# Kernel optimization log

Hardware: AMD Instinct MI355X
Metric: run time of the kernel (lower is better)

Reference implementation:

```python
import jax, jax.numpy as jnp
import numpy as np

N = 100000
E = 1600000
D_IN = 256
N_HEADS = 4
OUT_SZ = 32  # output_dim // n_heads = 128 // 4
ALPHA = 0.2  # leaky relu slope


def setup_inputs() -> dict:
    key = jax.random.key(0)
    ks = jax.random.split(key, 8)
    x = jax.random.normal(ks[0], (N, D_IN), dtype=jnp.float32)
    edge_row = jax.random.randint(ks[1], (E,), 0, N, dtype=jnp.int32)
    edge_col = jax.random.randint(ks[2], (E,), 0, N, dtype=jnp.int32)
    # per-head params: W (conv1d k=1, no bias), a1/a2 (conv1d k=1 with bias)
    W = jax.random.normal(ks[3], (N_HEADS, D_IN, OUT_SZ), dtype=jnp.float32) * (1.0 / np.sqrt(D_IN))
    a1 = jax.random.normal(ks[4], (N_HEADS, OUT_SZ), dtype=jnp.float32) * (1.0 / np.sqrt(OUT_SZ))
    b1 = jnp.zeros((N_HEADS,), dtype=jnp.float32)
    a2 = jax.random.normal(ks[5], (N_HEADS, OUT_SZ), dtype=jnp.float32) * (1.0 / np.sqrt(OUT_SZ))
    b2 = jnp.zeros((N_HEADS,), dtype=jnp.float32)
    return {"x": x, "W": W, "a1": a1, "b1": b1, "a2": a2, "b2": b2,
            "edge_row": edge_row, "edge_col": edge_col}


def _gat_heads(x, W, a1, b1, a2, b2, edge_row, edge_col):
    # per-head linear transform: [H, N, O]
    fts = jnp.einsum('nd,hdo->hno', x, W)
    f1 = jnp.einsum('hno,ho->hn', fts, a1) + b1[:, None]  # [H, N]
    f2 = jnp.einsum('hno,ho->hn', fts, a2) + b2[:, None]  # [H, N]
    # edge logits: f1[row] + f2[col]  (adj values are 1)
    logits = f1[:, edge_row] + f2[:, edge_col]            # [H, E]
    lr = jnp.maximum(ALPHA * logits, logits)
    # segment softmax over each node's incoming edge set (rows)
    seg_max = jax.vmap(lambda v: jax.ops.segment_max(v, edge_row, num_segments=N))(lr)
    ex = jnp.exp(lr - seg_max[:, edge_row])
    denom = jax.vmap(lambda v: jax.ops.segment_sum(v, edge_row, num_segments=N))(ex)
    coef = ex / denom[:, edge_row]                        # [H, E]
    # SpMM aggregation: out[h, i] = sum_{e: row(e)=i} coef[h,e] * fts[h, col(e)]
    msg = coef[:, :, None] * fts[:, edge_col, :]          # [H, E, O]
    agg = jax.vmap(lambda m: jax.ops.segment_sum(m, edge_row, num_segments=N))(msg)  # [H, N, O]
    h = jnp.transpose(agg, (1, 0, 2)).reshape(N, N_HEADS * OUT_SZ)  # concat heads
    return jax.nn.elu(h)[None]  # [1, N, output_dim]


def reference(x, W, a1, b1, a2, b2, edge_row, edge_col):
    return _gat_heads(x, W, a1, b1, a2, b2, edge_row, edge_col)
```

## Files before the change

### kernel.cpp

```cpp
#include <hip/hip_runtime.h>
#include <hip/hip_bf16.h>
#include <math.h>

#define ALPHA 0.2f
#define PB_EDGES 4096

typedef __attribute__((ext_vector_type(8))) short short8;
typedef __attribute__((ext_vector_type(4))) float floatx4;

__device__ __forceinline__ ushort f2bf(float f) {
    uint u = __float_as_uint(f);
    u += 0x7fff + ((u >> 16) & 1);
    return (ushort)(u >> 16);
}

__global__ __launch_bounds__(256) void k_wprep(const float* __restrict__ W,
                                               ushort* __restrict__ Wt)
{
    int g = blockIdx.x * 256 + threadIdx.x;
    int c = g >> 8, d = g & 255;
    Wt[g] = f2bf(W[(c >> 5) * 8192 + d * 32 + (c & 31)]);
}

__global__ __launch_bounds__(256) void k_gemm(const float* __restrict__ x,
                                              const ushort* __restrict__ Wt,
                                              const float* __restrict__ a1v,
                                              const float* __restrict__ b1v,
                                              const float* __restrict__ a2v,
                                              const float* __restrict__ b2v,
                                              ushort* __restrict__ fts2,
                                              float* __restrict__ f1,
                                              float* __restrict__ f2, int M)
{
    __shared__ __align__(16) ushort smem[64 * 264];
    const int t  = threadIdx.x;
    const int m0 = blockIdx.x * 64;

#pragma unroll
    for (int i = 0; i < 16; i++) {
        int idx = i * 256 + t;
        int row = idx >> 6, c4 = idx & 63;
        int gr = m0 + row;
        float4 v = make_float4(0.f, 0.f, 0.f, 0.f);
        if (gr < M) v = *(const float4*)(x + (size_t)gr * 256 + c4 * 4);
        ushort4 b;
        b.x = f2bf(v.x); b.y = f2bf(v.y); b.z = f2bf(v.z); b.w = f2bf(v.w);
        *(ushort4*)&smem[row * 264 + c4 * 4] = b;
    }
    __syncthreads();

    const int w = t >> 6, lane = t & 63;
    const int mm = lane & 15, qq = lane >> 4;

    floatx4 acc[8];
#pragma unroll
    for (int ct = 0; ct < 8; ct++) acc[ct] = (floatx4){0.f, 0.f, 0.f, 0.f};

    const ushort* arow = &smem[(16 * w + mm) * 264 + qq * 8];
#pragma unroll
    for (int ks = 0; ks < 8; ks++) {
        short8 a8 = *(const short8*)(arow + ks * 32);
#pragma unroll
        for (int ct = 0; ct < 8; ct++) {
            short8 b8 = *(const short8*)(Wt + (ct * 16 + mm) * 256 + ks * 32 + qq * 8);
            acc[ct] = __builtin_amdgcn_mfma_f32_16x16x32_bf16(a8, b8, acc[ct], 0, 0, 0);
        }
    }

    __syncthreads();
    ushort* ftsL = smem;
#pragma unroll
    for (int ct = 0; ct < 8; ct++) {
#pragma unroll
        for (int i = 0; i < 4; i++) {
            int row = 16 * w + qq * 4 + i;
            ftsL[row * 136 + ct * 16 + mm] = f2bf(acc[ct][i]);
        }
    }
    __syncthreads();

    {
        int row = t >> 2, q4 = t & 3;
        int gr = m0 + row;
        if (gr < M) {
            const uint4* src = (const uint4*)&ftsL[row * 136 + q4 * 32];
            uint4* dst = (uint4*)(fts2 + (size_t)gr * 128 + q4 * 32);
            dst[0] = src[0];
            dst[1] = src[1];
            dst[2] = src[2];
            dst[3] = src[3];
        }
    }
    {
        int row = t >> 2, h = t & 3;
        int gr = m0 + row;
        if (gr < M) {
            const ushort* fr = &ftsL[row * 136 + h * 32];
            float s1 = 0.f, s2 = 0.f;
#pragma unroll
            for (int o = 0; o < 32; o++) {
                float v = __uint_as_float((uint)fr[o] << 16);
                s1 = fmaf(v, a1v[h * 32 + o], s1);
                s2 = fmaf(v, a2v[h * 32 + o], s2);
            }
            f1[gr * 4 + h] = s1 + b1v[h];
            f2[gr * 4 + h] = s2 + b2v[h];
        }
    }
}

__global__ __launch_bounds__(256) void k_phist(const int* __restrict__ erow,
                                               int* __restrict__ bcnt, int E, int NB)
{
    __shared__ int h[512];
    for (int i = threadIdx.x; i < 512; i += 256) h[i] = 0;
    __syncthreads();
    int b0 = blockIdx.x * PB_EDGES;
    int bend = b0 + PB_EDGES; if (bend > E) bend = E;
    for (int j = b0 + threadIdx.x; j < bend; j += 256)
        atomicAdd(&h[erow[j] >> 8], 1);
    __syncthreads();
    for (int i = threadIdx.x; i < NB; i += 256)
        if (h[i]) atomicAdd(&bcnt[i], h[i]);
}

__global__ __launch_bounds__(256) void k_scan_buckets(const int* __restrict__ bcnt,
                                                      int* __restrict__ base,
                                                      int* __restrict__ bcursor,
                                                      int NB, int E)
{
    __shared__ int s[256];
    int t = threadIdx.x;
    int i0 = 2 * t, i1 = 2 * t + 1;
    int v0 = (i0 < NB) ? bcnt[i0] : 0;
    int v1 = (i1 < NB) ? bcnt[i1] : 0;
    int tsum = v0 + v1;
    s[t] = tsum;
    __syncthreads();
    for (int off = 1; off < 256; off <<= 1) {
        int u = (t >= off) ? s[t - off] : 0;
        __syncthreads();
        s[t] += u;
        __syncthreads();
    }
    int excl = s[t] - tsum;
    if (i0 < NB) { base[i0] = excl;      bcursor[i0] = excl; }
    if (i1 < NB) { base[i1] = excl + v0; bcursor[i1] = excl + v0; }
    if (t == 0) base[NB] = E;
}

__global__ __launch_bounds__(256) void k_pscatter(const int* __restrict__ erow,
                                                  const int* __restrict__ ecol,
                                                  int* __restrict__ bcursor,
                                                  uint* __restrict__ part, int E)
{
    __shared__ int h[512];
    __shared__ int cur[512];
    for (int i = threadIdx.x; i < 512; i += 256) h[i] = 0;
    __syncthreads();
    int b0 = blockIdx.x * PB_EDGES;
    int bend = b0 + PB_EDGES; if (bend > E) bend = E;
    for (int j = b0 + threadIdx.x; j < bend; j += 256)
        atomicAdd(&h[erow[j] >> 8], 1);
    __syncthreads();
    for (int i = threadIdx.x; i < 512; i += 256)
        cur[i] = h[i] ? atomicAdd(&bcursor[i], h[i]) : 0;
    __syncthreads();
    for (int j = b0 + threadIdx.x; j < bend; j += 256) {
        int r = erow[j], c = ecol[j];
        int p = atomicAdd(&cur[r >> 8], 1);
        part[p] = ((uint)(r & 255) << 24) | (uint)c;
    }
}

__global__ __launch_bounds__(256) void k_bucket(const uint* __restrict__ part,
                                                const int* __restrict__ base,
                                                int* __restrict__ row_start,
                                                int* __restrict__ col_sorted,
                                                int Nn, int NB, int E)
{
    __shared__ int cnt[256];
    __shared__ int s[256];
    __shared__ int cur[256];
    const int b = blockIdx.x, t = threadIdx.x;
    const int start = base[b], end = base[b + 1];

    cnt[t] = 0;
    __syncthreads();
    for (int j = start + t; j < end; j += 256)
        atomicAdd(&cnt[part[j] >> 24], 1);
    __syncthreads();
    int v = cnt[t];
    s[t] = v;
    __syncthreads();
    for (int off = 1; off < 256; off <<= 1) {
        int u = (t >= off) ? s[t - off] : 0;
        __syncthreads();
        s[t] += u;
        __syncthreads();
    }
    int excl = s[t] - v;
    int r = b * 256 + t;
    if (r < Nn) row_start[r] = start + excl;
    if (b == 0 && t == 0) row_start[Nn] = E;
    cur[t] = start + excl;
    __syncthreads();
    for (int j = start + t; j < end; j += 256) {
        uint rc = part[j];
        int p = atomicAdd(&cur[rc >> 24], 1);
        col_sorted[p] = (int)(rc & 0xffffffu);
    }
}

__global__ __launch_bounds__(256) void k_gat_row(const ushort* __restrict__ fts2,
                                                 const float4* __restrict__ f1,
                                                 const float4* __restrict__ f2,
                                                 const int* __restrict__ row_start,
                                                 const int* __restrict__ cols,
                                                 float* __restrict__ out, int Nn)
{
    __shared__ float eL[4][256];
    __shared__ int   cL[4][64];

    const int wid  = threadIdx.x >> 6;
    const int lane = threadIdx.x & 63;
    const int r = blockIdx.x * 4 + wid;
    if (r >= Nn) return;

    const int s = row_start[r], e = row_start[r + 1];
    const int hl = lane >> 4;

    float2* outp = (float2*)(out + (size_t)r * 128);
    if (s == e) { outp[lane] = make_float2(0.f, 0.f); return; }

    const float4 f1r = f1[r];
    float ds0 = 0.f, ds1 = 0.f, ds2 = 0.f, ds3 = 0.f;
    float acc0 = 0.f, acc1 = 0.f;

    for (int j0 = s; j0 < e; j0 += 64) {
        int j = j0 + lane;
        bool act = (j < e);
        int c = act ? cols[j] : 0;
        float4 f2v = f2[c];
        float l0 = f1r.x + f2v.x; l0 = fmaxf(l0, ALPHA * l0);
        float l1 = f1r.y + f2v.y; l1 = fmaxf(l1, ALPHA * l1);
        float l2 = f1r.z + f2v.z; l2 = fmaxf(l2, ALPHA * l2);
        float l3 = f1r.w + f2v.w; l3 = fmaxf(l3, ALPHA * l3);
        float e0 = act ? __expf(l0) : 0.f;
        float e1 = act ? __expf(l1) : 0.f;
        float e2 = act ? __expf(l2) : 0.f;
        float e3 = act ? __expf(l3) : 0.f;
        ds0 += e0; ds1 += e1; ds2 += e2; ds3 += e3;

        asm volatile("s_waitcnt lgkmcnt(0)" ::: "memory");
        ((float4*)eL[wid])[lane] = make_float4(e0, e1, e2, e3);
        cL[wid][lane] = c;
        asm volatile("s_waitcnt lgkmcnt(0)" ::: "memory");

        int len = e - j0; if (len > 64) len = 64;
#pragma unroll 4
        for (int jj = 0; jj < len; jj++) {
            float ee = eL[wid][jj * 4 + hl];
            int   cc = cL[wid][jj];
            const uint* fp = (const uint*)(fts2 + (size_t)cc * 128);
            uint vv = fp[lane];
            float vx = __uint_as_float(vv << 16);
            float vy = __uint_as_float(vv & 0xffff0000u);
            acc0 = fmaf(ee, vx, acc0);
            acc1 = fmaf(ee, vy, acc1);
        }
    }

#pragma unroll
    for (int off = 32; off > 0; off >>= 1) {
        ds0 += __shfl_xor(ds0, off, 64);
        ds1 += __shfl_xor(ds1, off, 64);
        ds2 += __shfl_xor(ds2, off, 64);
        ds3 += __shfl_xor(ds3, off, 64);
    }
    float dsel = (hl == 0) ? ds0 : (hl == 1) ? ds1 : (hl == 2) ? ds2 : ds3;

    float o0 = acc0 / dsel;
    float o1 = acc1 / dsel;
    o0 = (o0 > 0.f) ? o0 : (__expf(o0) - 1.0f);
    o1 = (o1 > 0.f) ? o1 : (__expf(o1) - 1.0f);
    outp[lane] = make_float2(o0, o1);
}

extern "C" void kernel_launch(void* const* d_in, const int* in_sizes, int n_in,
                              void* d_out, int out_size, void* d_ws, size_t ws_size,
                              hipStream_t stream)
{
    const float* x   = (const float*)d_in[0];
    const float* W   = (const float*)d_in[1];
    const float* a1  = (const float*)d_in[2];
    const float* b1  = (const float*)d_in[3];
    const float* a2  = (const float*)d_in[4];
    const float* b2  = (const float*)d_in[5];
    const int*   erow = (const int*)d_in[6];
    const int*   ecol = (const int*)d_in[7];
    float* out = (float*)d_out;

    const int N = in_sizes[0] / 256;
    const int E = in_sizes[6];
    const int NB = (N + 255) >> 8;

    char*  ws  = (char*)d_ws;
    size_t off = 0;
    auto carve = [&](size_t bytes) -> char* {
        char* p = ws + off;
        off += (bytes + 255) & ~(size_t)255;
        return p;
    };
    ushort* fts2      = (ushort*)carve((size_t)N * 128 * 2);
    ushort* Wt        = (ushort*)carve((size_t)128 * 256 * 2);
    float*  f1        = (float*)carve((size_t)N * 4 * 4);
    float*  f2        = (float*)carve((size_t)N * 4 * 4);
    int*    row_start = (int*)carve(((size_t)N + 1) * 4);
    int*    bcnt      = (int*)carve(512 * 4);
    int*    base      = (int*)carve(513 * 4);
    int*    bcursor   = (int*)carve(512 * 4);
    int*    col_sorted= (int*)carve((size_t)E * 4);
    uint*   part      = (uint*)carve((size_t)E * 4);
    (void)ws_size;

    k_wprep<<<128, 256, 0, stream>>>(W, Wt);
    k_gemm<<<(N + 63) / 64, 256, 0, stream>>>(x, Wt, a1, b1, a2, b2, fts2, f1, f2, N);

    hipMemsetAsync(bcnt, 0, 512 * 4, stream);
    int npb = (E + PB_EDGES - 1) / PB_EDGES;
    k_phist<<<npb, 256, 0, stream>>>(erow, bcnt, E, NB);
    k_scan_buckets<<<1, 256, 0, stream>>>(bcnt, base, bcursor, NB, E);
    k_pscatter<<<npb, 256, 0, stream>>>(erow, ecol, bcursor, part, E);
    k_bucket<<<NB, 256, 0, stream>>>(part, base, row_start, col_sorted, N, NB, E);

    k_gat_row<<<(N + 3) / 4, 256, 0, stream>>>(fts2, (const float4*)f1, (const float4*)f2,
                                               row_start, col_sorted, out, N);
}
```

Measured before the change: 382.4 us.

## Stage W in LDS and load x fragments directly into registers in GEMM

The GEMM kernel now processes 128 rows per block instead of 64. It stages the bf16 weight matrix in shared memory in MFMA fragment order, and each wave computes two 16-row tiles that reuse each B fragment. A fragments are loaded straight from global fp32 x into registers and converted there, skipping the LDS round trip for x. This cuts repeated global W reads and LDS traffic, at the cost of higher register use (two accumulator sets plus 16 A fragments), which may lower occupancy.

```diff
diff --git a/kernel.cpp b/kernel.cpp
--- a/kernel.cpp
+++ b/kernel.cpp
@@ -12,6 +12,15 @@
     uint u = __float_as_uint(f);
     u += 0x7fff + ((u >> 16) & 1);
     return (ushort)(u >> 16);
+}
+
+__device__ __forceinline__ short8 pack8(float4 lo, float4 hi) {
+    short8 r;
+    r[0] = (short)f2bf(lo.x); r[1] = (short)f2bf(lo.y);
+    r[2] = (short)f2bf(lo.z); r[3] = (short)f2bf(lo.w);
+    r[4] = (short)f2bf(hi.x); r[5] = (short)f2bf(hi.y);
+    r[6] = (short)f2bf(hi.z); r[7] = (short)f2bf(hi.w);
+    return r;
 }
 
 __global__ __launch_bounds__(256) void k_wprep(const float* __restrict__ W,
@@ -32,70 +41,87 @@
                                               float* __restrict__ f1,
                                               float* __restrict__ f2, int M)
 {
-    __shared__ __align__(16) ushort smem[64 * 264];
+    __shared__ __align__(16) ushort smem[32768];
     const int t  = threadIdx.x;
-    const int m0 = blockIdx.x * 64;
+    const int m0 = blockIdx.x * 128;
 
 #pragma unroll
     for (int i = 0; i < 16; i++) {
-        int idx = i * 256 + t;
-        int row = idx >> 6, c4 = idx & 63;
-        int gr = m0 + row;
-        float4 v = make_float4(0.f, 0.f, 0.f, 0.f);
-        if (gr < M) v = *(const float4*)(x + (size_t)gr * 256 + c4 * 4);
-        ushort4 b;
-        b.x = f2bf(v.x); b.y = f2bf(v.y); b.z = f2bf(v.z); b.w = f2bf(v.w);
-        *(ushort4*)&smem[row * 264 + c4 * 4] = b;
-    }
-    __syncthreads();
+        int f = i * 256 + t;
+        int lane_ = f & 63, ksct = f >> 6;
+        int ks = ksct & 7, ct = ksct >> 3;
+        int mm = lane_ & 15, qq = lane_ >> 4;
+        *(uint4*)&smem[f * 8] = *(const uint4*)&Wt[(ct * 16 + mm) * 256 + ks * 32 + qq * 8];
+    }
 
     const int w = t >> 6, lane = t & 63;
     const int mm = lane & 15, qq = lane >> 4;
 
-    floatx4 acc[8];
-#pragma unroll
-    for (int ct = 0; ct < 8; ct++) acc[ct] = (floatx4){0.f, 0.f, 0.f, 0.f};
-
-    const ushort* arow = &smem[(16 * w + mm) * 264 + qq * 8];
+    int row0 = m0 + w * 32 + mm;
+    int row1 = row0 + 16;
+    int r0c = (row0 < M) ? row0 : (M - 1);
+    int r1c = (row1 < M) ? row1 : (M - 1);
+    const float* ar0 = x + (size_t)r0c * 256 + qq * 8;
+    const float* ar1 = x + (size_t)r1c * 256 + qq * 8;
+    short8 afrag[2][8];
 #pragma unroll
     for (int ks = 0; ks < 8; ks++) {
-        short8 a8 = *(const short8*)(arow + ks * 32);
+        float4 lo0 = *(const float4*)(ar0 + ks * 32);
+        float4 hi0 = *(const float4*)(ar0 + ks * 32 + 4);
+        float4 lo1 = *(const float4*)(ar1 + ks * 32);
+        float4 hi1 = *(const float4*)(ar1 + ks * 32 + 4);
+        afrag[0][ks] = pack8(lo0, hi0);
+        afrag[1][ks] = pack8(lo1, hi1);
+    }
+
+    floatx4 acc[2][8];
+#pragma unroll
+    for (int r = 0; r < 2; r++)
+#pragma unroll
+        for (int ct = 0; ct < 8; ct++) acc[r][ct] = (floatx4){0.f, 0.f, 0.f, 0.f};
+
+    __syncthreads();
+
+#pragma unroll
+    for (int ks = 0; ks < 8; ks++) {
 #pragma unroll
         for (int ct = 0; ct < 8; ct++) {
-            short8 b8 = *(const short8*)(Wt + (ct * 16 + mm) * 256 + ks * 32 + qq * 8);
-            acc[ct] = __builtin_amdgcn_mfma_f32_16x16x32_bf16(a8, b8, acc[ct], 0, 0, 0);
+            short8 b8 = *(const short8*)&smem[((ct * 8 + ks) * 64 + lane) * 8];
+            acc[0][ct] = __builtin_amdgcn_mfma_f32_16x16x32_bf16(afrag[0][ks], b8, acc[0][ct], 0, 0, 0);
+            acc[1][ct] = __builtin_amdgcn_mfma_f32_16x16x32_bf16(afrag[1][ks], b8, acc[1][ct], 0, 0, 0);
         }
     }
 
     __syncthreads();
     ushort* ftsL = smem;
 #pragma unroll
-    for (int ct = 0; ct < 8; ct++) {
-#pragma unroll
-        for (int i = 0; i < 4; i++) {
-            int row = 16 * w + qq * 4 + i;
-            ftsL[row * 136 + ct * 16 + mm] = f2bf(acc[ct][i]);
+    for (int r = 0; r < 2; r++)
+#pragma unroll
+        for (int ct = 0; ct < 8; ct++)
+#pragma unroll
+            for (int i = 0; i < 4; i++) {
+                int rowl = w * 32 + r * 16 + qq * 4 + i;
+                ftsL[rowl * 136 + ct * 16 + mm] = f2bf(acc[r][ct][i]);
+            }
+    __syncthreads();
+
+    {
+        int rowl = t >> 1, half = t & 1;
+        int gr = m0 + rowl;
+        if (gr < M) {
+            const uint4* src = (const uint4*)&ftsL[rowl * 136 + half * 64];
+            uint4* dst = (uint4*)(fts2 + (size_t)gr * 128 + half * 64);
+#pragma unroll
+            for (int i = 0; i < 8; i++) dst[i] = src[i];
         }
     }
-    __syncthreads();
-
-    {
-        int row = t >> 2, q4 = t & 3;
-        int gr = m0 + row;
+#pragma unroll
+    for (int p = 0; p < 2; p++) {
+        int task = p * 256 + t;
+        int rowl = task >> 2, h = task & 3;
+        int gr = m0 + rowl;
         if (gr < M) {
-            const uint4* src = (const uint4*)&ftsL[row * 136 + q4 * 32];
-            uint4* dst = (uint4*)(fts2 + (size_t)gr * 128 + q4 * 32);
-            dst[0] = src[0];
-            dst[1] = src[1];
-            dst[2] = src[2];
-            dst[3] = src[3];
-        }
-    }
-    {
-        int row = t >> 2, h = t & 3;
-        int gr = m0 + row;
-        if (gr < M) {
-            const ushort* fr = &ftsL[row * 136 + h * 32];
+            const ushort* fr = &ftsL[rowl * 136 + h * 32];
             float s1 = 0.f, s2 = 0.f;
 #pragma unroll
             for (int o = 0; o < 32; o++) {
@@ -325,7 +351,7 @@
     (void)ws_size;
 
     k_wprep<<<128, 256, 0, stream>>>(W, Wt);
-    k_gemm<<<(N + 63) / 64, 256, 0, stream>>>(x, Wt, a1, b1, a2, b2, fts2, f1, f2, N);
+    k_gemm<<<(N + 127) / 128, 256, 0, stream>>>(x, Wt, a1, b1, a2, b2, fts2, f1, f2, N);
 
     hipMemsetAsync(bcnt, 0, 512 * 4, stream);
     int npb = (E + PB_EDGES - 1) / PB_EDGES;
```

New measurement: 340.7 us. 10.9% less time.
